# Performance work log

Hardware: AMD Instinct MI355X
Metric: run time of the kernel (lower is better)

Reference implementation:

```python
import jax, jax.numpy as jnp
import numpy as np

# Module hyperparameters (from init_kwargs)
MAX_D = 64      # maxDisplacement
PAD = 1         # zero padding on H and W
K = 3           # patch (kernel) size, odd
S_K = 1         # output spatial stride
S_D = 2         # displacement stride
EPS = 1e-8      # numerical guard for zero-norm patches


def setup_inputs() -> dict:
    key = jax.random.key(0)
    k0, k1 = jax.random.split(key)
    x0 = jax.random.normal(k0, (4, 64, 256, 512), dtype=jnp.float32)
    x1 = jax.random.normal(k1, (4, 64, 256, 512), dtype=jnp.float32)
    return {"x0": x0, "x1": x1}


def _box(a, k, s):
    # k x k box-sum over the last two dims with stride s, VALID.
    return jax.lax.reduce_window(a, 0.0, jax.lax.add, (1, k, k), (1, s, s), "VALID")


def _corr_zn(x0, x1):
    # Zero-normalized patch cross-correlation cost volume.
    # For each displacement d in {-MAX_D, ..., +MAX_D} step S_D (along W):
    #   v0 = KxK x C patch of x0 at (y, x); v1 = patch of x1 at (y, x + d)
    #   C[b, d, y, x] = <v0 - mean(v0), v1 - mean(v1)> / (||v0 - m0|| * ||v1 - m1|| + eps)
    # Implemented via box filters: dot(v0, v1) = boxsum_k(sum_c x0 * shift_d(x1)),
    # mean/norm from boxsums of x and x^2.
    B, C, H, W = x0.shape
    n = float(C * K * K)  # patch element count
    p = PAD
    x0p = jnp.pad(x0, ((0, 0), (0, 0), (p, p), (p, p)))
    x1p = jnp.pad(x1, ((0, 0), (0, 0), (p, p), (p, p)))
    Wp = W + 2 * p
    # Pad x1 along W by MAX_D on both sides so every shift is a static-size slice.
    x1pad = jnp.pad(x1p, ((0, 0), (0, 0), (0, 0), (MAX_D, MAX_D)))

    # x0 patch statistics (shared across displacements): (B, Ho, Wo)
    s0 = _box(x0p.sum(1), K, S_K)                 # sum of patch elements
    sq0 = _box((x0p * x0p).sum(1), K, S_K)        # sum of squares
    L0 = jnp.sqrt(jnp.maximum(sq0 - s0 * s0 / n, 0.0))  # centered L2 norm

    nD = 2 * (MAX_D // S_D) + 1
    offsets = jnp.arange(nD, dtype=jnp.int32) * S_D  # slice starts into x1pad

    def body(carry, off):
        x1s = jax.lax.dynamic_slice_in_dim(x1pad, off, Wp, axis=3)  # x1 shifted by d = off - MAX_D
        s1 = _box(x1s.sum(1), K, S_K)
        sq1 = _box((x1s * x1s).sum(1), K, S_K)
        L1 = jnp.sqrt(jnp.maximum(sq1 - s1 * s1 / n, 0.0))
        dot = _box((x0p * x1s).sum(1), K, S_K)
        numer = dot - s0 * s1 / n  # centered dot product
        c = numer / (L0 * L1 + EPS)
        return carry, c

    _, cs = jax.lax.scan(body, None, offsets)  # (nD, B, Ho, Wo)
    return jnp.transpose(cs, (1, 0, 2, 3))     # (B, nD, Ho, Wo)


def reference(x0, x1):
    return _corr_zn(x0, x1)
```

## Files before the change

kernel.cpp:

```cpp
#include <hip/hip_runtime.h>

typedef __attribute__((ext_vector_type(8))) short bf16x8_t;
typedef __attribute__((ext_vector_type(4))) float f32x4_t;
typedef __attribute__((ext_vector_type(4))) unsigned u32x4_t;
typedef unsigned int u32;

#define BATCH 4
#define CH 64
#define HIN 256
#define WIN 512
#define NDISP 65
#define TY 2
#define TX 254
#define NSTEP 8

#define CS0_OFF 0
#define CQ0_OFF  524288
#define CS1_OFF 1048576
#define CQ1_OFF 1572864
#define SB0_OFF 2097152
#define LB0_OFF 2621440
#define SB1_OFF 3145728
#define LB1_OFF 3809280
#define STATS_FLOATS 4472832UL
#define X1T_U16 33554432UL
#define WS_NEED_BYTES (STATS_FLOATS*4UL + 2UL*X1T_U16*2UL)

#define BUFB 43008
#define X0PARB 8192
#define X1SEC 16384
#define X1PARB 13312
#define SM_S0X 129024
#define SM_L0X 130048
#define SM_S1X 131072
#define SM_L1X 132608
#define SMEMB 134144

#define FB_BUF 40960
#define FB_X0 0
#define FB_X0PS 8192
#define FB_X1 16384
#define FB_X1PS 12288
#define FB_QB 0
#define FB_S0X 66824
#define FB_L0X 67848
#define FB_S1X 68872
#define FB_L1X 70408
#define FB_SMEM 81920

#define WAITVM(n) asm volatile("s_waitcnt vmcnt(" #n ")" ::: "memory")

__device__ __forceinline__ void gl16(const void* g, void* l) {
  __builtin_amdgcn_global_load_lds(
      (const __attribute__((address_space(1))) u32*)g,
      (__attribute__((address_space(3))) u32*)l, 16, 0, 0);
}

__device__ __forceinline__ int fixog(int og, int xb, int ogmax) {
  const int xmin = xb + 32 * og;
  if (xmin + 30 < 0 || xmin >= WIN) {
    int f = (31 - xb) >> 5;
    f = f < 0 ? 0 : f;
    og = f > ogmax ? ogmax : f;
  }
  return og;
}

__global__ __launch_bounds__(512)
void colsum_kernel(const float* __restrict__ x0, const float* __restrict__ x1,
                   float* __restrict__ ws, int write_t) {
  const int y = blockIdx.x, b = blockIdx.y, x = threadIdx.x;
  const size_t plane = (size_t)HIN * WIN;
  const float* p0 = x0 + (size_t)b * CH * plane + (size_t)y * WIN + x;
  const float* p1 = x1 + (size_t)b * CH * plane + (size_t)y * WIN + x;
  unsigned short* t0 = (unsigned short*)(ws + STATS_FLOATS);
  unsigned short* t1 = t0 + X1T_U16;
  float s0 = 0.f, q0 = 0.f, s1 = 0.f, q1 = 0.f;
  for (int cc = 0; cc < 2; ++cc) {
    u32 w0[16], w1[16];
#pragma unroll
    for (int j = 0; j < 16; ++j) {
      const float a0 = p0[(size_t)(cc * 32 + 2 * j) * plane];
      const float a1 = p0[(size_t)(cc * 32 + 2 * j + 1) * plane];
      const float c0 = p1[(size_t)(cc * 32 + 2 * j) * plane];
      const float c1 = p1[(size_t)(cc * 32 + 2 * j + 1) * plane];
      s0 += a0 + a1; q0 += a0 * a0 + a1 * a1;
      s1 += c0 + c1; q1 += c0 * c0 + c1 * c1;
      asm("v_cvt_pk_bf16_f32 %0, %1, %2" : "=v"(w0[j]) : "v"(a0), "v"(a1));
      asm("v_cvt_pk_bf16_f32 %0, %1, %2" : "=v"(w1[j]) : "v"(c0), "v"(c1));
    }
    if (write_t) {
      const size_t o = ((((size_t)b * 2 + cc) * HIN + y) * WIN + x) * 32;
#pragma unroll
      for (int g = 0; g < 4; ++g) {
        u32x4_t v0 = {w0[4*g], w0[4*g+1], w0[4*g+2], w0[4*g+3]};
        u32x4_t v1 = {w1[4*g], w1[4*g+1], w1[4*g+2], w1[4*g+3]};
        *(u32x4_t*)(t0 + o + 8 * g) = v0;
        *(u32x4_t*)(t1 + o + 8 * g) = v1;
      }
    }
  }
  const size_t o = ((size_t)b * HIN + y) * WIN + x;
  ws[CS0_OFF + o] = s0; ws[CQ0_OFF + o] = q0;
  ws[CS1_OFF + o] = s1; ws[CQ1_OFF + o] = q1;
}

__global__ __launch_bounds__(512)
void boxnorm_kernel(float* __restrict__ ws) {
  const int y = blockIdx.x, b = blockIdx.y;
  const int tid = threadIdx.x;
  const float invn = 1.f / 576.f;
  const int ylo = (y > 0) ? y - 1 : 0;
  const int yhi = (y < HIN - 1) ? y + 1 : HIN - 1;
  {
    const int x = tid;
    float s = 0.f, q = 0.f;
    for (int yy = ylo; yy <= yhi; ++yy) {
      const float* rs = ws + CS0_OFF + ((size_t)b * HIN + yy) * WIN;
      const float* rq = ws + CQ0_OFF + ((size_t)b * HIN + yy) * WIN;
      const int xlo = (x > 0) ? x - 1 : 0;
      const int xhi = (x < WIN - 1) ? x + 1 : WIN - 1;
      for (int xx = xlo; xx <= xhi; ++xx) { s += rs[xx]; q += rq[xx]; }
    }
    const size_t o = ((size_t)b * HIN + y) * WIN + x;
    ws[SB0_OFF + o] = s;
    ws[LB0_OFF + o] = sqrtf(fmaxf(q - s * s * invn, 0.f));
  }
  for (int i = tid; i < 648; i += 512) {
    const int v = i - 66;
    float s = 0.f, q = 0.f;
    const int xlo = (v - 1 > 0) ? v - 1 : 0;
    const int xhi = (v + 1 < WIN - 1) ? v + 1 : WIN - 1;
    if (v + 1 >= 0 && v - 1 < WIN) {
      for (int yy = ylo; yy <= yhi; ++yy) {
        const float* rs = ws + CS1_OFF + ((size_t)b * HIN + yy) * WIN;
        const float* rq = ws + CQ1_OFF + ((size_t)b * HIN + yy) * WIN;
        for (int xx = xlo; xx <= xhi; ++xx) { s += rs[xx]; q += rq[xx]; }
      }
    }
    const size_t o = ((size_t)b * HIN + y) * 648 + i;
    ws[SB1_OFF + o] = s;
    ws[LB1_OFF + o] = sqrtf(fmaxf(q - s * s * invn, 0.f));
  }
}

__global__ __launch_bounds__(1024, 4)
void corrzn_dma_kernel(const float* __restrict__ ws, float* __restrict__ out) {
  __shared__ __align__(16) char smem[SMEMB];

  const int tid  = threadIdx.x;
  const int lane = tid & 63;
  const int wv   = tid >> 6;
  const int p    = wv & 1;
  const int ch   = wv >> 1;
  const int lm = lane & 15;
  const int lk = lane >> 4;

  const int flat = blockIdx.x + 3 * (blockIdx.y + 128 * blockIdx.z);
  const int sw = (flat & 7) * 192 + (flat >> 3);
  const int bx = sw % 3;
  const int tmp = sw / 3;
  const int by = tmp & 127;
  const int b  = tmp >> 7;

  const int x0blk = bx * TX;
  const int y0    = by * TY;

  const unsigned short* t0 = (const unsigned short*)(ws + STATS_FLOATS);
  const unsigned short* t1 = t0 + X1T_U16;

  const int pa  = wv >> 3, ga0 = wv & 7;
  const int xbA = x0blk - 1 + pa;
  const int gaA = fixog(ga0, xbA, 7);
  const int pb  = (wv >= 13) ? 1 : 0;
  const int xbB = x0blk - 65 + pb;
  const int gaB = fixog(wv - 13 * pb, xbB, 12);
  const int xbC = x0blk - 64;
  const int gaC = fixog(wv + 3, xbC, 12);

  f32x4_t acc[TY][5];
#pragma unroll
  for (int t = 0; t < TY; ++t)
#pragma unroll
    for (int T = 0; T < 5; ++T)
      acc[t][T] = (f32x4_t){0.f, 0.f, 0.f, 0.f};

  auto issue = [&](int k) {
    const int r = k >> 1, cc = k & 1;
    int orow = y0 + r - 1;
    orow = orow < 0 ? 0 : (orow > HIN - 1 ? HIN - 1 : orow);
    char* bb = smem + (k % 3) * BUFB;
    const size_t rowo = ((((size_t)b * 2 + cc) * HIN + orow) * (size_t)WIN) * 32;
    const unsigned short* r0 = t0 + rowo;
    const unsigned short* r1 = t1 + rowo;
    {
      const int line = 16 * gaA + (lane >> 2);
      const int xg = xbA + 2 * line;
      const int ss = (lane & 3) ^ ((line >> 1) & 3);
      if (xg >= 0 && xg < WIN)
        gl16(r0 + (size_t)xg * 32 + ss * 8, bb + pa * X0PARB + gaA * 1024);
    }
    {
      const int line = 16 * gaB + (lane >> 2);
      const int xg = xbB + 2 * line;
      const int ss = (lane & 3) ^ ((line >> 1) & 3);
      if (xg >= 0 && xg < WIN)
        gl16(r1 + (size_t)xg * 32 + ss * 8, bb + X1SEC + pb * X1PARB + gaB * 1024);
    }
    if (wv < 10) {
      const int line = 16 * gaC + (lane >> 2);
      const int xg = xbC + 2 * line;
      const int ss = (lane & 3) ^ ((line >> 1) & 3);
      if (xg >= 0 && xg < WIN)
        gl16(r1 + (size_t)xg * 32 + ss * 8, bb + X1SEC + X1PARB + gaC * 1024);
    }
  };

  {
    u32x4_t z = {0u, 0u, 0u, 0u};
    for (int i = tid; i < 3 * BUFB / 16; i += 1024)
      ((u32x4_t*)smem)[i] = z;
  }
  __syncthreads();

  issue(0); issue(1); issue(2);
  if (wv < 10) { WAITVM(6); } else { WAITVM(4); }
  __builtin_amdgcn_s_barrier();
  asm volatile("" ::: "memory");

#pragma unroll
  for (int k = 0; k < NSTEP; ++k) {
    const int r = k >> 1;
    const int orow = y0 + r - 1;
    if (orow >= 0 && orow < HIN) {
      char* bb = smem + (k % 3) * BUFB;
      bf16x8_t afr, bfr[5];
      {
        const int pos = 16 * ch + lm;
        const int slot = lk ^ ((pos >> 1) & 3);
        afr = *(const bf16x8_t*)(bb + p * X0PARB + pos * 64 + slot * 16);
      }
#pragma unroll
      for (int T = 0; T < 5; ++T) {
        const int pos = 16 * (ch + T) + lm;
        const int slot = lk ^ ((pos >> 1) & 3);
        bfr[T] = *(const bf16x8_t*)(bb + X1SEC + p * X1PARB + pos * 64 + slot * 16);
      }
#pragma unroll
      for (int t = 0; t < TY; ++t) {
        if (t >= r - 2 && t <= r) {
#pragma unroll
          for (int T = 0; T < 5; ++T)
            acc[t][T] = __builtin_amdgcn_mfma_f32_16x16x32_bf16(
                afr, bfr[T], acc[t][T], 0, 0, 0);
        }
      }
    }
    asm volatile("s_waitcnt lgkmcnt(0)" ::: "memory");
    __builtin_amdgcn_s_barrier();
    asm volatile("" ::: "memory");
    if (k == NSTEP - 1) break;
    if (k + 3 < NSTEP) issue(k + 3);
    const int rem = (NSTEP - 2) - k;
    const int m = rem < 2 ? rem : 2;
    if (wv < 10) {
      if (m == 2) { WAITVM(6); } else if (m == 1) { WAITVM(3); } else { WAITVM(0); }
    } else {
      if (m == 2) { WAITVM(4); } else if (m == 1) { WAITVM(2); } else { WAITVM(0); }
    }
    __builtin_amdgcn_s_barrier();
    asm volatile("" ::: "memory");
  }

  float* Q   = (float*)(smem);
  float* s0x = (float*)(smem + SM_S0X);
  float* l0x = (float*)(smem + SM_L0X);
  float* s1x = (float*)(smem + SM_S1X);
  float* l1x = (float*)(smem + SM_L1X);
  const float invn = 1.f / 576.f;

#pragma unroll
  for (int t = 0; t < TY; ++t) {
    const int row = y0 + t;
    __syncthreads();
    for (int i = tid; i < 254; i += 1024) {
      const int x = x0blk + i;
      const size_t o = ((size_t)b * HIN + row) * WIN + x;
      s0x[i] = (x < WIN) ? ws[SB0_OFF + o] : 0.f;
      l0x[i] = (x < WIN) ? ws[LB0_OFF + o] : 0.f;
    }
    for (int j2 = tid; j2 < 382; j2 += 1024) {
      const int idx = x0blk + 2 + j2;
      const size_t o = ((size_t)b * HIN + row) * 648 + idx;
      s1x[j2] = (idx < 648) ? ws[SB1_OFF + o] : 0.f;
      l1x[j2] = (idx < 648) ? ws[LB1_OFF + o] : 0.f;
    }
#pragma unroll
    for (int T = 0; T < 5; ++T)
#pragma unroll
      for (int q = 0; q < 4; ++q) {
        const int mg = 16 * ch + lk * 4 + q;
        const int di = 16 * T + lm - 4 * lk - q;
        if (di >= 0 && di <= 64)
          Q[di * 257 + 2 * mg + p] = acc[t][T][q];
      }
    __syncthreads();
    for (int oi = tid; oi < NDISP * TX; oi += 1024) {
      const int di = oi / TX;
      const int xl = oi - di * TX;
      const int x = x0blk + xl;
      if (x < WIN) {
        const float q3 = Q[di * 257 + xl] + Q[di * 257 + xl + 1] + Q[di * 257 + xl + 2];
        const int j = xl + 2 * di;
        const float numer = q3 - s0x[xl] * s1x[j] * invn;
        const float den = l0x[xl] * l1x[j] + 1e-8f;
        float rd;
        asm("v_rcp_f32 %0, %1" : "=v"(rd) : "v"(den));
        out[(((size_t)b * NDISP + di) * HIN + row) * WIN + x] = numer * rd;
      }
    }
  }
}

__global__ __launch_bounds__(512, 2)
void corrzn_kernel(const float* __restrict__ x0, const float* __restrict__ x1,
                   const float* __restrict__ ws, float* __restrict__ out) {
  __shared__ __align__(16) char smem[FB_SMEM];
  const int tid  = threadIdx.x;
  const int lane = tid & 63;
  const int wv   = tid >> 6;
  const int p    = wv & 1;
  const int chunk0 = 2 * (wv >> 1);
  const int lm = lane & 15;
  const int lk = lane >> 4;
  const int t5  = tid & 31;
  const int cpx = tid >> 5;
  const int x0blk = blockIdx.x * TX;
  const int y0    = blockIdx.y * TY;
  const int b     = blockIdx.z;
  const size_t plane = (size_t)HIN * WIN;
  const float* x0b = x0 + (size_t)b * CH * plane;
  const float* x1b = x1 + (size_t)b * CH * plane;

  f32x4_t acc[TY][2][5];
#pragma unroll
  for (int t = 0; t < TY; ++t)
#pragma unroll
    for (int mc = 0; mc < 2; ++mc)
#pragma unroll
      for (int T = 0; T < 5; ++T)
        acc[t][mc][T] = (f32x4_t){0.f, 0.f, 0.f, 0.f};

  float2 R0[12], R1[12];
  auto prefetch = [&](int k) {
    const int r = k >> 1, cc = k & 1;
    const int orow = y0 + r - 1;
    const bool rowok = (orow >= 0) && (orow < HIN);
    const int ro = rowok ? orow : 0;
    const float* s0p = x0b + (size_t)(cc * 32 + 2 * cpx) * plane + (size_t)ro * WIN;
    const float* s1p = x1b + (size_t)(cc * 32 + 2 * cpx) * plane + (size_t)ro * WIN;
#pragma unroll
    for (int it = 0; it < 5; ++it) {
      const int wp = 32 * it + t5;
      const int xg = x0blk - 2 + 2 * wp;
      float2 a = {0.f, 0.f}, c = {0.f, 0.f};
      if (rowok && wp <= 128 && xg >= 0 && xg < WIN - 1) {
        a = *(const float2*)(s0p + xg);
        c = *(const float2*)(s0p + plane + xg);
      }
      R0[it] = a; R1[it] = c;
    }
#pragma unroll
    for (int it = 0; it < 7; ++it) {
      const int wp = 32 * it + t5;
      const int xg = x0blk - 66 + 2 * wp;
      float2 a = {0.f, 0.f}, c = {0.f, 0.f};
      if (rowok && wp <= 192 && xg >= 0 && xg < WIN - 1) {
        a = *(const float2*)(s1p + xg);
        c = *(const float2*)(s1p + plane + xg);
      }
      R0[5 + it] = a; R1[5 + it] = c;
    }
  };
  auto wstage = [&](int bb) {
#pragma unroll
    for (int it = 0; it < 12; ++it) {
      const bool isx1 = it >= 5;
      const int wp = 32 * (isx1 ? it - 5 : it) + t5;
      const int base = bb + (isx1 ? FB_X1 : FB_X0);
      const int ps   = isx1 ? FB_X1PS : FB_X0PS;
      const int pmax = isx1 ? 192 : 128;
      u32 pkA, pkB;
      asm("v_cvt_pk_bf16_f32 %0, %1, %2" : "=v"(pkA) : "v"(R0[it].x), "v"(R1[it].x));
      asm("v_cvt_pk_bf16_f32 %0, %1, %2" : "=v"(pkB) : "v"(R0[it].y), "v"(R1[it].y));
      if (wp >= 1 && wp <= pmax) {
        const int pos = wp - 1;
        const int slot = (cpx >> 2) ^ ((pos >> 1) & 3);
        *(u32*)(smem + base + ps + pos * 64 + slot * 16 + (cpx & 3) * 4) = pkA;
      }
      if (wp <= pmax - 1) {
        const int pos = wp;
        const int slot = (cpx >> 2) ^ ((pos >> 1) & 3);
        *(u32*)(smem + base + pos * 64 + slot * 16 + (cpx & 3) * 4) = pkB;
      }
    }
  };

  prefetch(0); wstage(0); prefetch(1);
  asm volatile("s_waitcnt lgkmcnt(0)" ::: "memory");
  __builtin_amdgcn_s_barrier();
  asm volatile("" ::: "memory");

#pragma unroll
  for (int k = 0; k < 12; ++k) {
    const int r = k >> 1;
    const int cur = (k & 1) * FB_BUF;
    bf16x8_t afr[2], bfr[6];
#pragma unroll
    for (int mc = 0; mc < 2; ++mc) {
      const int pos = 16 * (chunk0 + mc) + lm;
      const int slot = lk ^ ((pos >> 1) & 3);
      afr[mc] = *(const bf16x8_t*)(smem + cur + FB_X0 + p * FB_X0PS + pos * 64 + slot * 16);
    }
#pragma unroll
    for (int u = 0; u < 6; ++u) {
      const int pos = 16 * (chunk0 + u) + lm;
      const int slot = lk ^ ((pos >> 1) & 3);
      bfr[u] = *(const bf16x8_t*)(smem + cur + FB_X1 + p * FB_X1PS + pos * 64 + slot * 16);
    }
#pragma unroll
    for (int t = 0; t < TY; ++t) {
      if (t >= r - 2 && t <= r) {
#pragma unroll
        for (int mc = 0; mc < 2; ++mc)
#pragma unroll
          for (int T = 0; T < 5; ++T)
            acc[t][mc][T] = __builtin_amdgcn_mfma_f32_16x16x32_bf16(
                afr[mc], bfr[mc + T], acc[t][mc][T], 0, 0, 0);
      }
    }
    if (k < 11) {
      wstage(((k + 1) & 1) * FB_BUF);
      if (k + 2 < 12) prefetch(k + 2);
      asm volatile("s_waitcnt lgkmcnt(0)" ::: "memory");
      __builtin_amdgcn_s_barrier();
      asm volatile("" ::: "memory");
    }
  }

  float* Q   = (float*)(smem + FB_QB);
  float* s0x = (float*)(smem + FB_S0X);
  float* l0x = (float*)(smem + FB_L0X);
  float* s1x = (float*)(smem + FB_S1X);
  float* l1x = (float*)(smem + FB_L1X);
  const float invn = 1.f / 576.f;
#pragma unroll
  for (int t = 0; t < TY; ++t) {
    const int row = y0 + t;
    __syncthreads();
    for (int i = tid; i < 254; i += 512) {
      const int x = x0blk + i;
      const size_t o = ((size_t)b * HIN + row) * WIN + x;
      s0x[i] = (x < WIN) ? ws[SB0_OFF + o] : 0.f;
      l0x[i] = (x < WIN) ? ws[LB0_OFF + o] : 0.f;
    }
    for (int j2 = tid; j2 < 382; j2 += 512) {
      const int idx = x0blk + 2 + j2;
      const size_t o = ((size_t)b * HIN + row) * 648 + idx;
      s1x[j2] = (idx < 648) ? ws[SB1_OFF + o] : 0.f;
      l1x[j2] = (idx < 648) ? ws[LB1_OFF + o] : 0.f;
    }
#pragma unroll
    for (int mc = 0; mc < 2; ++mc)
#pragma unroll
      for (int T = 0; T < 5; ++T)
#pragma unroll
        for (int q = 0; q < 4; ++q) {
          const int mg = 16 * (chunk0 + mc) + lk * 4 + q;
          const int di = 16 * T + lm - 4 * lk - q;
          if (di >= 0 && di <= 64)
            Q[di * 257 + 2 * mg + p] = acc[t][mc][T][q];
        }
    __syncthreads();
    for (int oi = tid; oi < NDISP * TX; oi += 512) {
      const int di = oi / TX;
      const int xl = oi - di * TX;
      const int x = x0blk + xl;
      if (x < WIN) {
        const float q3 = Q[di * 257 + xl] + Q[di * 257 + xl + 1] + Q[di * 257 + xl + 2];
        const int j = xl + 2 * di;
        const float numer = q3 - s0x[xl] * s1x[j] * invn;
        const float den = l0x[xl] * l1x[j] + 1e-8f;
        float rd;
        asm("v_rcp_f32 %0, %1" : "=v"(rd) : "v"(den));
        out[(((size_t)b * NDISP + di) * HIN + row) * WIN + x] = numer * rd;
      }
    }
  }
}

extern "C" void kernel_launch(void* const* d_in, const int* in_sizes, int n_in,
                              void* d_out, int out_size, void* d_ws, size_t ws_size,
                              hipStream_t stream) {
  const float* x0 = (const float*)d_in[0];
  const float* x1 = (const float*)d_in[1];
  float* out = (float*)d_out;
  float* wsf = (float*)d_ws;
  const int use_dma = (ws_size >= WS_NEED_BYTES) ? 1 : 0;

  colsum_kernel<<<dim3(HIN, BATCH), 512, 0, stream>>>(x0, x1, wsf, use_dma);
  boxnorm_kernel<<<dim3(HIN, BATCH), 512, 0, stream>>>(wsf);
  if (use_dma) {
    corrzn_dma_kernel<<<dim3(3, HIN / TY, BATCH), 1024, 0, stream>>>(wsf, out);
  } else {
    corrzn_kernel<<<dim3(3, HIN / TY, BATCH), 512, 0, stream>>>(x0, x1, wsf, out);
  }
}
```

Before: 226.5 us.

## Shrink DMA kernel LDS to double buffering and vectorize epilogue stores

The DMA-based correlation kernel moves from triple to double buffering of the x0/x1 tiles, with smaller buffer sections and shifted stats-scratch offsets. This cuts LDS per block from about 131KB to 80KB, and the launch-bound hint rises from 4 to 8. The wave-to-load assignment and vmcnt waits are reworked for the new prefetch depth of two. The epilogue now has each thread compute two adjacent x outputs per displacement, sharing Q loads and writing float2, which removes per-element integer division. The cost is less prefetch depth to hide global-load latency.

```diff
diff --git a/kernel.cpp b/kernel.cpp
--- a/kernel.cpp
+++ b/kernel.cpp
@@ -26,15 +26,15 @@
 #define X1T_U16 33554432UL
 #define WS_NEED_BYTES (STATS_FLOATS*4UL + 2UL*X1T_U16*2UL)
 
-#define BUFB 43008
+#define BUFB 40960
 #define X0PARB 8192
 #define X1SEC 16384
-#define X1PARB 13312
-#define SM_S0X 129024
-#define SM_L0X 130048
-#define SM_S1X 131072
-#define SM_L1X 132608
-#define SMEMB 134144
+#define X1PARB 12288
+#define SM_S0X 66824
+#define SM_L0X 67848
+#define SM_S1X 68872
+#define SM_L1X 70408
+#define SMEMB 81920
 
 #define FB_BUF 40960
 #define FB_X0 0
@@ -144,7 +144,7 @@
   }
 }
 
-__global__ __launch_bounds__(1024, 4)
+__global__ __launch_bounds__(1024, 8)
 void corrzn_dma_kernel(const float* __restrict__ ws, float* __restrict__ out) {
   __shared__ __align__(16) char smem[SMEMB];
 
@@ -172,11 +172,12 @@
   const int pa  = wv >> 3, ga0 = wv & 7;
   const int xbA = x0blk - 1 + pa;
   const int gaA = fixog(ga0, xbA, 7);
-  const int pb  = (wv >= 13) ? 1 : 0;
+  const int pb  = (wv >= 12) ? 1 : 0;
   const int xbB = x0blk - 65 + pb;
-  const int gaB = fixog(wv - 13 * pb, xbB, 12);
+  const int gaB = fixog(wv - 12 * pb, xbB, 11);
   const int xbC = x0blk - 64;
-  const int gaC = fixog(wv + 3, xbC, 12);
+  const int gaC = fixog(wv + 4, xbC, 11);
+  const bool ops3 = (wv < 8);
 
   f32x4_t acc[TY][5];
 #pragma unroll
@@ -189,7 +190,7 @@
     const int r = k >> 1, cc = k & 1;
     int orow = y0 + r - 1;
     orow = orow < 0 ? 0 : (orow > HIN - 1 ? HIN - 1 : orow);
-    char* bb = smem + (k % 3) * BUFB;
+    char* bb = smem + (k & 1) * BUFB;
     const size_t rowo = ((((size_t)b * 2 + cc) * HIN + orow) * (size_t)WIN) * 32;
     const unsigned short* r0 = t0 + rowo;
     const unsigned short* r1 = t1 + rowo;
@@ -207,7 +208,7 @@
       if (xg >= 0 && xg < WIN)
         gl16(r1 + (size_t)xg * 32 + ss * 8, bb + X1SEC + pb * X1PARB + gaB * 1024);
     }
-    if (wv < 10) {
+    if (ops3) {
       const int line = 16 * gaC + (lane >> 2);
       const int xg = xbC + 2 * line;
       const int ss = (lane & 3) ^ ((line >> 1) & 3);
@@ -218,13 +219,13 @@
 
   {
     u32x4_t z = {0u, 0u, 0u, 0u};
-    for (int i = tid; i < 3 * BUFB / 16; i += 1024)
+    for (int i = tid; i < 2 * BUFB / 16; i += 1024)
       ((u32x4_t*)smem)[i] = z;
   }
   __syncthreads();
 
-  issue(0); issue(1); issue(2);
-  if (wv < 10) { WAITVM(6); } else { WAITVM(4); }
+  issue(0); issue(1);
+  if (ops3) { WAITVM(3); } else { WAITVM(2); }
   __builtin_amdgcn_s_barrier();
   asm volatile("" ::: "memory");
 
@@ -233,7 +234,7 @@
     const int r = k >> 1;
     const int orow = y0 + r - 1;
     if (orow >= 0 && orow < HIN) {
-      char* bb = smem + (k % 3) * BUFB;
+      char* bb = smem + (k & 1) * BUFB;
       bf16x8_t afr, bfr[5];
       {
         const int pos = 16 * ch + lm;
@@ -260,13 +261,11 @@
     __builtin_amdgcn_s_barrier();
     asm volatile("" ::: "memory");
     if (k == NSTEP - 1) break;
-    if (k + 3 < NSTEP) issue(k + 3);
-    const int rem = (NSTEP - 2) - k;
-    const int m = rem < 2 ? rem : 2;
-    if (wv < 10) {
-      if (m == 2) { WAITVM(6); } else if (m == 1) { WAITVM(3); } else { WAITVM(0); }
+    if (k + 2 < NSTEP) {
+      issue(k + 2);
+      if (ops3) { WAITVM(3); } else { WAITVM(2); }
     } else {
-      if (m == 2) { WAITVM(4); } else if (m == 1) { WAITVM(2); } else { WAITVM(0); }
+      WAITVM(0);
     }
     __builtin_amdgcn_s_barrier();
     asm volatile("" ::: "memory");
@@ -305,18 +304,24 @@
           Q[di * 257 + 2 * mg + p] = acc[t][T][q];
       }
     __syncthreads();
-    for (int oi = tid; oi < NDISP * TX; oi += 1024) {
-      const int di = oi / TX;
-      const int xl = oi - di * TX;
-      const int x = x0blk + xl;
-      if (x < WIN) {
-        const float q3 = Q[di * 257 + xl] + Q[di * 257 + xl + 1] + Q[di * 257 + xl + 2];
+    const int xl = 2 * (tid & 127);
+    const int di0 = tid >> 7;
+    if (xl < TX && x0blk + xl + 1 < WIN) {
+      for (int di = di0; di < NDISP; di += 8) {
+        const float qa0 = Q[di * 257 + xl];
+        const float qa1 = Q[di * 257 + xl + 1];
+        const float qa2 = Q[di * 257 + xl + 2];
+        const float qa3 = Q[di * 257 + xl + 3];
         const int j = xl + 2 * di;
-        const float numer = q3 - s0x[xl] * s1x[j] * invn;
-        const float den = l0x[xl] * l1x[j] + 1e-8f;
-        float rd;
-        asm("v_rcp_f32 %0, %1" : "=v"(rd) : "v"(den));
-        out[(((size_t)b * NDISP + di) * HIN + row) * WIN + x] = numer * rd;
+        const float n0 = (qa0 + qa1 + qa2) - s0x[xl] * s1x[j] * invn;
+        const float d0 = l0x[xl] * l1x[j] + 1e-8f;
+        const float n1 = (qa1 + qa2 + qa3) - s0x[xl + 1] * s1x[j + 1] * invn;
+        const float d1 = l0x[xl + 1] * l1x[j + 1] + 1e-8f;
+        float r0, r1;
+        asm("v_rcp_f32 %0, %1" : "=v"(r0) : "v"(d0));
+        asm("v_rcp_f32 %0, %1" : "=v"(r1) : "v"(d1));
+        float2 o2; o2.x = n0 * r0; o2.y = n1 * r1;
+        *(float2*)(out + (((size_t)b * NDISP + di) * HIN + row) * WIN + x0blk + xl) = o2;
       }
     }
   }
```

After: 256.3 us. +13.1%, slower.
